# Optimization experiments

Hardware: AMD Instinct MI355X
Metric: run time of the kernel (lower is better)

Reference implementation:

```python
import jax, jax.numpy as jnp
import numpy as np

NUM_HEADS = 8
WS1, WS2 = 3, 5
SR = 8
RES = 56
DIM = 256


def _normalize(x, axis=-1, eps=1e-12):
    n = jnp.linalg.norm(x, axis=axis, keepdims=True)
    return x / jnp.maximum(n, eps)


def _unfold(img, ws):
    # img: (B, C, H, W) -> (B, C, ws*ws, H*W), torch nn.Unfold ordering
    B, C, H, W = img.shape
    p = ws // 2
    pad = jnp.pad(img, ((0, 0), (0, 0), (p, p), (p, p)))
    cols = jnp.stack([pad[:, :, i:i + H, j:j + W]
                      for i in range(ws) for j in range(ws)], axis=2)
    return cols.reshape(B, C, ws * ws, H * W)


def _local_mask(H, W, ws):
    # True where the unfolded window position falls on zero padding; shape (N, ws*ws)
    ones = jnp.ones((1, 1, H, W), jnp.float32)
    cols = _unfold(ones, ws)[0, 0]            # (ws*ws, N)
    return cols.T == 0                         # (N, ws*ws)


def _layernorm(x, g, b, eps=1e-5):
    mu = x.mean(-1, keepdims=True)
    var = ((x - mu) ** 2).mean(-1, keepdims=True)
    return (x - mu) * jax.lax.rsqrt(var + eps) * g + b


def setup_inputs() -> dict:
    key = jax.random.key(0)
    ks = jax.random.split(key, 8)
    C, B, N = DIM, 4, RES * RES
    hd = C // NUM_HEADS

    def nrm(k, shape, s=0.02):
        return jax.random.normal(k, shape, jnp.float32) * s

    return {
        "x": jax.random.normal(ks[0], (B, N, C), jnp.float32),
        "Wq": nrm(ks[1], (C, C)), "bq": jnp.zeros((C,), jnp.float32),
        "Wkv": nrm(ks[2], (C, 2 * C)), "bkv": jnp.zeros((2 * C,), jnp.float32),
        "Wsr": nrm(ks[3], (C, C)), "bsr": jnp.zeros((C,), jnp.float32),
        "ln_g": jnp.ones((C,), jnp.float32), "ln_b": jnp.zeros((C,), jnp.float32),
        "tok1": nrm(ks[4], (NUM_HEADS, hd, WS1 * WS1)),
        "bias1": jnp.zeros((NUM_HEADS, 1, WS1 * WS1), jnp.float32),
        "tok2": nrm(ks[5], (NUM_HEADS, hd, WS2 * WS2)),
        "bias2": jnp.zeros((NUM_HEADS, 1, WS2 * WS2), jnp.float32),
        "Wproj": nrm(ks[6], (C, C)), "bproj": jnp.zeros((C,), jnp.float32),
        "patch_size": 56,
    }


def reference(x, Wq, bq, Wkv, bkv, Wsr, bsr, ln_g, ln_b,
              tok1, bias1, tok2, bias2, Wproj, bproj, patch_size):
    H = W = int(patch_size)
    B, N, C = x.shape
    h = NUM_HEADS
    d = C // h
    l1, l2 = WS1 * WS1, WS2 * WS2

    # queries, cosine-normalized per head
    q = (x @ Wq + bq).reshape(B, N, h, d).transpose(0, 2, 1, 3)   # (B,h,N,d)
    qn = _normalize(q)

    # shared kv projection (torch computes it twice with identical result)
    kv = x @ Wkv + bkv
    k, v = kv[..., :C], kv[..., C:]
    kn = _normalize(k.reshape(B, N, h, d)).reshape(B, N, C)
    kv_img = jnp.concatenate([kn, v], axis=-1).transpose(0, 2, 1).reshape(B, 2 * C, H, W)

    def local_branch(ws):
        l = ws * ws
        cols = _unfold(kv_img, ws)                                # (B,2C,l,N)
        cols = cols.reshape(B, 2 * h, d, l, N).transpose(0, 1, 4, 2, 3)  # (B,2h,N,d,l)
        kl, vl = cols[:, :h], cols[:, h:]
        a = jnp.einsum('bhnd,bhndl->bhnl', qn, kl)
        a = jnp.where(_local_mask(H, W, ws)[None, None], -jnp.inf, a)
        return a, vl

    a1, vl1 = local_branch(WS1)
    a2, vl2 = local_branch(WS2)

    # pooled global branch
    x_img = x.transpose(0, 2, 1).reshape(B, C, H, W)
    x_sr = jnp.einsum('bchw,oc->bohw', x_img, Wsr.T.T) if False else jnp.einsum('bchw,co->bohw', x_img, Wsr) + bsr[None, :, None, None]
    x_sr = jax.nn.gelu(x_sr, approximate=False)
    pH, pW = H // SR, W // SR
    pooled = x_sr.reshape(B, C, pH, SR, pW, SR).mean(axis=(3, 5))  # adaptive avg pool
    P = pH * pW
    x_p = pooled.reshape(B, C, P).transpose(0, 2, 1)               # (B,P,C)
    x_p = _layernorm(x_p, ln_g, ln_b)
    kvp = (x_p @ Wkv + bkv).reshape(B, P, 2 * h, d).transpose(0, 2, 1, 3)
    kp, vp = kvp[:, :h], kvp[:, h:]
    ap = jnp.einsum('bhnd,bhpd->bhnp', qn, _normalize(kp))

    # joint softmax over both local windows and pooled tokens
    attn = jax.nn.softmax(jnp.concatenate([a1, a2, ap], axis=-1), axis=-1)
    s1 = attn[..., :l1]
    s2 = attn[..., l1:l1 + l2]
    sp = attn[..., l1 + l2:]

    x1 = jnp.einsum('bhnl,bhndl->bhnd',
                    jnp.einsum('bhnd,hdl->bhnl', qn, tok1) + bias1[None] + s1, vl1)
    x2 = jnp.einsum('bhnl,bhndl->bhnd',
                    jnp.einsum('bhnd,hdl->bhnl', qn, tok2) + bias2[None] + s2, vl2)
    xp = jnp.einsum('bhnp,bhpd->bhnd', sp, vp)

    out = (x1 + x2 + xp).transpose(0, 2, 1, 3).reshape(B, N, C)
    return out @ Wproj + bproj
```

## Files before the change

kernel.cpp:

```cpp
#include <hip/hip_runtime.h>
#include <hip/hip_bf16.h>

using bf16 = __hip_bfloat16;

#define B_  4
#define H_  56
#define W_  56
#define N_  3136
#define C_  256
#define NH  8
#define HD  32
#define P_  49
#define PH  7
#define TOKC 272
#define KS2  136

typedef __attribute__((ext_vector_type(8))) short short8;
typedef __attribute__((ext_vector_type(4))) float f32x4;

__device__ __forceinline__ float bfu2f(ushort u) { return __uint_as_float((uint32_t)u << 16); }
__device__ __forceinline__ ushort f2bf_u(float f) {
    uint32_t u = __float_as_uint(f);
    uint32_t r = (u + 0x7FFFu + ((u >> 16) & 1u)) >> 16;
    return (ushort)r;
}
__device__ __forceinline__ uint32_t pk2(float a, float b) {
    return (uint32_t)f2bf_u(a) | ((uint32_t)f2bf_u(b) << 16);
}
__device__ __forceinline__ float lo16(uint32_t u) { return __uint_as_float(u << 16); }
__device__ __forceinline__ float hi16(uint32_t u) { return __uint_as_float(u & 0xffff0000u); }

__device__ __forceinline__ float half_reduce(float v) {
#pragma unroll
    for (int m = 16; m >= 1; m >>= 1) v += __shfl_xor(v, m);
    return v;
}

__device__ __forceinline__ float block_sum(float val, float* red) {
#pragma unroll
    for (int m = 32; m >= 1; m >>= 1) val += __shfl_xor(val, m);
    __syncthreads();
    if ((threadIdx.x & 63) == 0) red[threadIdx.x >> 6] = val;
    __syncthreads();
    return red[0] + red[1] + red[2] + red[3];
}

__global__ __launch_bounds__(256) void k_prep(
    const float* __restrict__ Wq, const float* __restrict__ Wkv,
    const float* __restrict__ Wsr, const float* __restrict__ Wproj,
    const float* __restrict__ tok1, const float* __restrict__ bias1,
    const float* __restrict__ tok2, const float* __restrict__ bias2,
    ushort* __restrict__ WT, ushort* __restrict__ WTp,
    ushort* __restrict__ TD, float* __restrict__ biasT)
{
    const int gid = blockIdx.x * 256 + threadIdx.x;
    const int gs = gridDim.x * 256;
    for (int i = gid; i < 1024 * 256; i += gs) {
        int o = i >> 8, c = i & 255;
        float w = (o < 256) ? Wq[c * 256 + o]
                : (o < 768) ? Wkv[c * 512 + (o - 256)]
                            : Wsr[c * 256 + (o - 768)];
        WT[i] = f2bf_u(w);
    }
    for (int i = gid; i < 256 * 256; i += gs) {
        int o = i >> 8, c = i & 255;
        WTp[i] = f2bf_u(Wproj[c * 256 + o]);
    }
    for (int i = gid; i < 320 * 256; i += gs) {
        int j = i >> 8, k = i & 255;
        float val = 0.f;
        if (j < TOKC) {
            int h = j / 34, l = j % 34;
            if ((k >> 5) == h) {
                int d = k & 31;
                val = (l < 9) ? tok1[(h * HD + d) * 9 + l]
                              : tok2[(h * HD + d) * 25 + (l - 9)];
            }
        }
        TD[i] = f2bf_u(val);
    }
    for (int i = gid; i < 320; i += gs) {
        float bv = 0.f;
        if (i < TOKC) {
            int h = i / 34, l = i % 34;
            bv = (l < 9) ? bias1[h * 9 + l] : bias2[h * 25 + (l - 9)];
        }
        biasT[i] = bv;
    }
}

__global__ __launch_bounds__(256) void k_gemm_in(
    const float* __restrict__ xf,
    const ushort* __restrict__ WT,
    const float* __restrict__ bq, const float* __restrict__ bkv,
    const float* __restrict__ bsr,
    ushort* __restrict__ qnu,
    ushort* __restrict__ knu, ushort* __restrict__ vu, ushort* __restrict__ srgu)
{
    const int r0 = blockIdx.x * 64;
    const int halfy = blockIdx.y;
    const int t = threadIdx.x;
    __shared__ __align__(16) ushort As[64 * 264];
    __shared__ __align__(16) ushort Bs[64 * 264];

#pragma unroll
    for (int i = 0; i < 8; i++) {
        int chunk = t + i * 256;
        int row = chunk >> 5, ks8 = (chunk & 31) * 8;
        const float* src = xf + (size_t)(r0 + row) * 256 + ks8;
        float4 f0 = *(const float4*)(src);
        float4 f1 = *(const float4*)(src + 4);
        uint4 o;
        o.x = pk2(f0.x, f0.y); o.y = pk2(f0.z, f0.w);
        o.z = pk2(f1.x, f1.y); o.w = pk2(f1.z, f1.w);
        *(uint4*)(As + row * 264 + ks8) = o;
    }
    __syncthreads();

    const int w = t >> 6, lane = t & 63;
    const int arow = w * 16 + (lane & 15);
    const int k0 = (lane >> 4) * 8;
    const int colq = lane & 15;
    const int rb = r0 + w * 16 + (lane >> 4) * 4;

    short8 areg[8];
#pragma unroll
    for (int kk = 0; kk < 8; kk++)
        areg[kk] = *(const short8*)(As + arow * 264 + kk * 32 + k0);

    for (int cc = 0; cc < 8; cc++) {
        const int cb = halfy * 512 + cc * 64;
        const int mode = cb >> 8;
        const int cm = cb & 255;

        __syncthreads();
#pragma unroll
        for (int i = 0; i < 8; i++) {
            int chunk = t + i * 256;
            int row = chunk >> 5, ks8 = (chunk & 31) * 8;
            *(uint4*)(Bs + row * 264 + ks8) =
                *(const uint4*)(WT + (size_t)(cb + row) * 256 + ks8);
        }
        __syncthreads();

        f32x4 acc[4];
#pragma unroll
        for (int ct = 0; ct < 4; ct++) acc[ct] = (f32x4){0.f, 0.f, 0.f, 0.f};
#pragma unroll
        for (int kk = 0; kk < 8; kk++) {
#pragma unroll
            for (int ct = 0; ct < 4; ct++) {
                short8 b = *(const short8*)(Bs + (ct * 16 + colq) * 264 + kk * 32 + k0);
                acc[ct] = __builtin_amdgcn_mfma_f32_16x16x32_bf16(areg[kk], b, acc[ct], 0, 0, 0);
            }
        }

        const float* bp = (mode == 0) ? bq : (mode == 1) ? bkv : (mode == 2) ? (bkv + 256) : bsr;
#pragma unroll
        for (int ct = 0; ct < 4; ct++) {
            float bv = bp[cm + ct * 16 + colq];
#pragma unroll
            for (int j = 0; j < 4; j++) acc[ct][j] += bv;
        }

        if (mode <= 1) {
#pragma unroll
            for (int hp = 0; hp < 2; hp++) {
#pragma unroll
                for (int j = 0; j < 4; j++) {
                    float ss = acc[2 * hp][j] * acc[2 * hp][j] + acc[2 * hp + 1][j] * acc[2 * hp + 1][j];
                    ss += __shfl_xor(ss, 1); ss += __shfl_xor(ss, 2);
                    ss += __shfl_xor(ss, 4); ss += __shfl_xor(ss, 8);
                    float inv = 1.0f / fmaxf(sqrtf(ss), 1e-12f);
                    acc[2 * hp][j] *= inv; acc[2 * hp + 1][j] *= inv;
                }
            }
        } else if (mode == 3) {
#pragma unroll
            for (int ct = 0; ct < 4; ct++)
#pragma unroll
                for (int j = 0; j < 4; j++) {
                    float s = acc[ct][j];
                    acc[ct][j] = 0.5f * s * (1.0f + erff(s * 0.70710678118654752f));
                }
        }

#pragma unroll
        for (int ct = 0; ct < 4; ct++) {
            int gcol = cm + ct * 16 + colq;
#pragma unroll
            for (int j = 0; j < 4; j++) {
                float vvv = acc[ct][j];
                size_t ro = (size_t)(rb + j);
                if (mode == 0)      qnu[ro * 256 + gcol] = f2bf_u(vvv);
                else if (mode == 1) knu[ro * 256 + gcol] = f2bf_u(vvv);
                else if (mode == 2) vu[ro * 256 + gcol] = f2bf_u(vvv);
                else                srgu[ro * 256 + gcol] = f2bf_u(vvv);
            }
        }
    }
}

template <int MODE>
__global__ __launch_bounds__(256) void k_gemm(
    const ushort* __restrict__ Abf,
    const ushort* __restrict__ WT,
    const float*  __restrict__ bias,
    float* __restrict__ dstF,
    ushort* __restrict__ dstT)
{
    const int r0 = blockIdx.x * 64;
    const int cb = blockIdx.y * 64;
    const int t = threadIdx.x;
    __shared__ __align__(16) ushort As[64 * 264];
    __shared__ __align__(16) ushort Bs[64 * 264];

#pragma unroll
    for (int i = 0; i < 8; i++) {
        int chunk = t + i * 256;
        int row = chunk >> 5, ks = (chunk & 31) * 8;
        *(uint4*)(As + row * 264 + ks) = *(const uint4*)(Abf + (size_t)(r0 + row) * 256 + ks);
        *(uint4*)(Bs + row * 264 + ks) = *(const uint4*)(WT + (size_t)(cb + row) * 256 + ks);
    }
    __syncthreads();

    const int w = t >> 6, lane = t & 63;
    const int arow = w * 16 + (lane & 15);
    const int k0 = (lane >> 4) * 8;
    f32x4 acc[4];
#pragma unroll
    for (int ct = 0; ct < 4; ct++) acc[ct] = (f32x4){0.f, 0.f, 0.f, 0.f};

#pragma unroll
    for (int kk = 0; kk < 8; kk++) {
        short8 a = *(const short8*)(As + arow * 264 + kk * 32 + k0);
#pragma unroll
        for (int ct = 0; ct < 4; ct++) {
            short8 b = *(const short8*)(Bs + (ct * 16 + (lane & 15)) * 264 + kk * 32 + k0);
            acc[ct] = __builtin_amdgcn_mfma_f32_16x16x32_bf16(a, b, acc[ct], 0, 0, 0);
        }
    }

    const int colq = lane & 15;
    const int rb = r0 + w * 16 + (lane >> 4) * 4;
#pragma unroll
    for (int ct = 0; ct < 4; ct++) {
        float bv = bias[cb + ct * 16 + colq];
#pragma unroll
        for (int j = 0; j < 4; j++) acc[ct][j] += bv;
    }

#pragma unroll
    for (int ct = 0; ct < 4; ct++) {
        int gcol = cb + ct * 16 + colq;
#pragma unroll
        for (int j = 0; j < 4; j++) {
            if (MODE == 4) {
                dstF[(size_t)(rb + j) * 256 + gcol] = acc[ct][j];
            } else {
                if (gcol < TOKC)
                    dstT[(size_t)(rb + j) * TOKC + gcol] = f2bf_u(acc[ct][j]);
            }
        }
    }
}

__global__ __launch_bounds__(256) void k_srt(
    const uint32_t* __restrict__ srgu32,
    const float* __restrict__ Wkv, const float* __restrict__ bkv,
    const float* __restrict__ ln_g, const float* __restrict__ ln_b,
    ushort* __restrict__ kpn_u, ushort* __restrict__ vpu)
{
    const int cell = blockIdx.x;
    const int b = cell / P_, p = cell % P_;
    const int py = p / PH, px = p % PH;
    const int t = threadIdx.x;
    const int ph = t >> 7, cp = t & 127;
    __shared__ float xp[C_];
    __shared__ float red[4];

    float sx = 0.f, sy = 0.f;
    for (int k = 0; k < 32; k++) {
        int pi = ph * 32 + k;
        int n = (py * 8 + (pi >> 3)) * W_ + px * 8 + (pi & 7);
        uint32_t u = srgu32[((size_t)b * N_ + n) * 128 + cp];
        sx += lo16(u); sy += hi16(u);
    }
    if (ph == 1) { xp[2 * cp] = sx; xp[2 * cp + 1] = sy; }
    __syncthreads();
    if (ph == 0) {
        xp[2 * cp]     = (xp[2 * cp] + sx) * (1.0f / 64.0f);
        xp[2 * cp + 1] = (xp[2 * cp + 1] + sy) * (1.0f / 64.0f);
    }
    __syncthreads();

    float acc = xp[t];
    float mean = block_sum(acc, red) * (1.0f / C_);
    float dv = acc - mean;
    float var = block_sum(dv * dv, red) * (1.0f / C_);
    float xpv = dv * rsqrtf(var + 1e-5f) * ln_g[t] + ln_b[t];
    __syncthreads();
    xp[t] = xpv;
    __syncthreads();

    float ak = bkv[t];
    float av = bkv[C_ + t];
    for (int c = 0; c < C_; c++) {
        float xv = xp[c];
        ak += xv * Wkv[c * 2 * C_ + t];
        av += xv * Wkv[c * 2 * C_ + C_ + t];
    }
    float nk = fmaxf(sqrtf(half_reduce(ak * ak)), 1e-12f);
    size_t o = (size_t)cell * C_ + t;
    kpn_u[o] = f2bf_u(ak / nk);
    vpu[o]  = f2bf_u(av);
}

__global__ __launch_bounds__(256) void k_qkav(
    const ushort* __restrict__ qnu,
    const uint32_t* __restrict__ knu,
    const uint32_t* __restrict__ vu,
    const ushort* __restrict__ kpnu,
    const ushort* __restrict__ vpu,
    const ushort* __restrict__ tokcu,
    uint32_t* __restrict__ pre_bfu)
{
    const int tile = blockIdx.x;
    const int b  = blockIdx.y >> 1;
    const int hs = blockIdx.y & 1;
    const int ty = tile / 14, tx = tile % 14;
    const int t = threadIdx.x;
    __shared__ __align__(16) ushort ks[64 * KS2];
    __shared__ ushort coefS[16 * 4 * 80];
    __shared__ ushort tokcS[16 * 136];

    uint32_t* ks32 = (uint32_t*)ks;
    for (int idx = t; idx < 64 * 32; idx += 256) {
        int r = idx >> 5, u2 = idx & 31;
        int gy = ty * 4 + (r >> 3) - 2, gx = tx * 4 + (r & 7) - 2;
        uint2 kv = make_uint2(0u, 0u);
        if (gy >= 0 && gy < H_ && gx >= 0 && gx < W_) {
            size_t base = ((size_t)b * N_ + gy * W_ + gx) * 128 + hs * 64 + 2 * u2;
            kv = *reinterpret_cast<const uint2*>(knu + base);
        }
        ks32[r * (KS2 / 2) + 2 * u2]     = kv.x;
        ks32[r * (KS2 / 2) + 2 * u2 + 1] = kv.y;
    }
    {
        uint32_t* tokcS32 = (uint32_t*)tokcS;
        const uint32_t* tsrc = (const uint32_t*)tokcu;
        for (int idx = t; idx < 16 * 68; idx += 256) {
            int tk = idx / 68, d = idx % 68;
            size_t flat = (size_t)b * N_ + (ty * 4 + (tk >> 2)) * W_ + tx * 4 + (tk & 3);
            tokcS32[tk * 68 + d] = tsrc[flat * 136 + hs * 68 + d];
        }
    }
    __syncthreads();

    const int w = t >> 6, lane = t & 63;
    const int h = hs * 4 + w;
    const int col = lane & 15, kslc = lane >> 4;

    int r8[4], c8[4]; bool inb[4]; int pcl[4]; bool pval[4];
#pragma unroll
    for (int ct = 0; ct < 4; ct++) {
        int key = ct * 16 + col;
        r8[ct] = key >> 3; c8[ct] = key & 7;
        int gy = ty * 4 + r8[ct] - 2, gx = tx * 4 + c8[ct] - 2;
        inb[ct] = (gy >= 0) && (gy < H_) && (gx >= 0) && (gx < W_);
        pval[ct] = key < P_;
        pcl[ct] = pval[ct] ? key : (P_ - 1);
    }

    size_t aflat = (size_t)b * N_ + (ty * 4 + (col >> 2)) * W_ + tx * 4 + (col & 3);
    short8 a = *(const short8*)(qnu + aflat * 256 + h * 32 + kslc * 8);

    f32x4 aw[4], ap[4];
#pragma unroll
    for (int ct = 0; ct < 4; ct++) {
        short8 bw = *(const short8*)(ks + (ct * 16 + col) * KS2 + w * 32 + kslc * 8);
        aw[ct] = __builtin_amdgcn_mfma_f32_16x16x32_bf16(a, bw, (f32x4){0.f,0.f,0.f,0.f}, 0, 0, 0);
        short8 bp = *(const short8*)(kpnu + ((size_t)b * P_ + pcl[ct]) * 256 + h * 32 + kslc * 8);
        ap[ct] = __builtin_amdgcn_mfma_f32_16x16x32_bf16(a, bp, (f32x4){0.f,0.f,0.f,0.f}, 0, 0, 0);
    }

#pragma unroll
    for (int j = 0; j < 4; j++) {
        float mj = -INFINITY;
#pragma unroll
        for (int ct = 0; ct < 4; ct++) {
            int dy = r8[ct] - kslc - 2, dx = c8[ct] - j - 2;
            bool win = inb[ct] && dy >= -2 && dy <= 2 && dx >= -2 && dx <= 2;
            if (win) mj = fmaxf(mj, aw[ct][j]);
            if (pval[ct]) mj = fmaxf(mj, ap[ct][j]);
        }
        mj = fmaxf(mj, __shfl_xor(mj, 1)); mj = fmaxf(mj, __shfl_xor(mj, 2));
        mj = fmaxf(mj, __shfl_xor(mj, 4)); mj = fmaxf(mj, __shfl_xor(mj, 8));
        float ej = 0.f;
        float ew[4], ep[4];
#pragma unroll
        for (int ct = 0; ct < 4; ct++) {
            int dy = r8[ct] - kslc - 2, dx = c8[ct] - j - 2;
            bool win = inb[ct] && dy >= -2 && dy <= 2 && dx >= -2 && dx <= 2;
            bool inner = dy >= -1 && dy <= 1 && dx >= -1 && dx <= 1;
            ew[ct] = win ? (inner ? 2.0f : 1.0f) * __expf(aw[ct][j] - mj) : 0.f;
            ep[ct] = pval[ct] ? __expf(ap[ct][j] - mj) : 0.f;
            ej += ew[ct] + ep[ct];
        }
        ej += __shfl_xor(ej, 1); ej += __shfl_xor(ej, 2);
        ej += __shfl_xor(ej, 4); ej += __shfl_xor(ej, 8);
        float sc = 1.0f / ej;
        const ushort* tokc_j = tokcS + (kslc * 4 + j) * 136 + w * 34;
        ushort* coefT = coefS + ((kslc * 4 + j) * 4 + w) * 80;
#pragma unroll
        for (int ct = 0; ct < 4; ct++) {
            int dy = r8[ct] - kslc - 2, dx = c8[ct] - j - 2;
            if (dy >= -2 && dy <= 2 && dx >= -2 && dx <= 2) {
                bool inner = dy >= -1 && dy <= 1 && dx >= -1 && dx <= 1;
                int l25 = (dy + 2) * 5 + (dx + 2);
                float tm = bfu2f(tokc_j[9 + l25]);
                if (inner) tm += bfu2f(tokc_j[(dy + 1) * 3 + (dx + 1)]);
                coefT[l25] = f2bf_u(ew[ct] * sc + tm);
            }
            if (pval[ct]) coefT[25 + ct * 16 + col] = f2bf_u(ep[ct] * sc);
        }
    }
    __syncthreads();

    const int tk = t >> 4, g = t & 15;
    const int iy = tk >> 2, ix = tk & 3;
    const int y = ty * 4 + iy, x = tx * 4 + ix;
    const size_t pflat = (size_t)b * N_ + y * W_ + x;
    const ushort* cf = coefS + (tk * 4 + (g >> 2)) * 80;

    float a0x = 0.f, a0y = 0.f, a1x = 0.f, a1y = 0.f;
    float a2x = 0.f, a2y = 0.f, a3x = 0.f, a3y = 0.f;

#pragma unroll 5
    for (int l = 0; l < 25; l++) {
        int dy = l / 5 - 2, dx = l % 5 - 2;
        int yy = y + dy, xx2 = x + dx;
        if (yy < 0 || yy >= H_ || xx2 < 0 || xx2 >= W_) continue;
        float wc = bfu2f(cf[l]);
        uint4 vv = *reinterpret_cast<const uint4*>(
            vu + ((size_t)b * N_ + yy * W_ + xx2) * 128 + hs * 64 + g * 4);
        a0x += wc * lo16(vv.x); a0y += wc * hi16(vv.x);
        a1x += wc * lo16(vv.y); a1y += wc * hi16(vv.y);
        a2x += wc * lo16(vv.z); a2y += wc * hi16(vv.z);
        a3x += wc * lo16(vv.w); a3y += wc * hi16(vv.w);
    }
#pragma unroll 7
    for (int p = 0; p < 49; p++) {
        float wc = bfu2f(cf[25 + p]);
        uint4 vv = *reinterpret_cast<const uint4*>(
            (const uint32_t*)vpu + ((size_t)b * P_ + p) * 128 + hs * 64 + g * 4);
        a0x += wc * lo16(vv.x); a0y += wc * hi16(vv.x);
        a1x += wc * lo16(vv.y); a1y += wc * hi16(vv.y);
        a2x += wc * lo16(vv.z); a2y += wc * hi16(vv.z);
        a3x += wc * lo16(vv.w); a3y += wc * hi16(vv.w);
    }
    uint4 o;
    o.x = pk2(a0x, a0y);
    o.y = pk2(a1x, a1y);
    o.z = pk2(a2x, a2y);
    o.w = pk2(a3x, a3y);
    *reinterpret_cast<uint4*>(pre_bfu + pflat * 128 + hs * 64 + g * 4) = o;
}

extern "C" void kernel_launch(void* const* d_in, const int* in_sizes, int n_in,
                              void* d_out, int out_size, void* d_ws, size_t ws_size,
                              hipStream_t stream)
{
    (void)in_sizes; (void)n_in; (void)out_size; (void)ws_size;
    const float* x     = (const float*)d_in[0];
    const float* Wq    = (const float*)d_in[1];
    const float* bq    = (const float*)d_in[2];
    const float* Wkv   = (const float*)d_in[3];
    const float* bkv   = (const float*)d_in[4];
    const float* Wsr   = (const float*)d_in[5];
    const float* bsr   = (const float*)d_in[6];
    const float* ln_g  = (const float*)d_in[7];
    const float* ln_b  = (const float*)d_in[8];
    const float* tok1  = (const float*)d_in[9];
    const float* bias1 = (const float*)d_in[10];
    const float* tok2  = (const float*)d_in[11];
    const float* bias2 = (const float*)d_in[12];
    const float* Wproj = (const float*)d_in[13];
    const float* bproj = (const float*)d_in[14];
    float* out = (float*)d_out;

    const size_t nhalf = (size_t)B_ * N_ * 128;

    uint32_t* vu     = (uint32_t*)d_ws;
    uint32_t* knu    = vu + nhalf;
    uint32_t* srgu   = knu + nhalf;
    uint32_t* qnu32  = srgu + nhalf;
    ushort*   WTus   = (ushort*)(qnu32 + nhalf);
    ushort*   WTpus  = WTus + 1024 * 256;
    ushort*   TDus   = WTpus + 256 * 256;
    float*    biasT  = (float*)(TDus + 320 * 256);
    ushort*   vpu    = (ushort*)(biasT + 320);
    uint32_t* kpnu   = (uint32_t*)(vpu + (size_t)B_ * P_ * 256);

    ushort* qnu   = (ushort*)qnu32;
    ushort* tokcu = (ushort*)d_out;

    k_prep<<<512, 256, 0, stream>>>(Wq, Wkv, Wsr, Wproj, tok1, bias1, tok2, bias2,
                                    WTus, WTpus, TDus, biasT);
    k_gemm_in<<<dim3(196, 2), 256, 0, stream>>>(x, WTus, bq, bkv, bsr,
                                                qnu, (ushort*)knu,
                                                (ushort*)vu, (ushort*)srgu);
    k_gemm<5><<<dim3(196, 5), 256, 0, stream>>>(qnu, TDus, biasT, nullptr, tokcu);
    k_srt<<<B_ * P_, 256, 0, stream>>>(srgu, Wkv, bkv, ln_g, ln_b, (ushort*)kpnu, vpu);
    k_qkav<<<dim3(196, B_ * 2), 256, 0, stream>>>(qnu, knu, vu, (const ushort*)kpnu,
                                                  vpu, tokcu, srgu);
    k_gemm<4><<<dim3(196, 4), 256, 0, stream>>>((ushort*)srgu, WTpus, bproj, out, nullptr);
}
```

Baseline: 128.6 us.

## Compute attention-weighted V aggregation with MFMA using padded channel-major V layout

The scalar per-thread gather of 25 local V neighbours and 49 pooled V tokens is replaced by MFMA matrix multiplies. V is now stored channel-major in a zero-padded spatial grid, and pooled V is stored transposed and padded to 64. This lets coefficient tiles in shared memory multiply against contiguous V rows. The aim is to cut scalar FMA and uncoalesced-load cost in the aggregation step. In exchange, the prep kernel must zero a large padded buffer and the V write in the GEMM epilogue becomes strided scatter.

```diff
diff --git a/kernel.cpp b/kernel.cpp
--- a/kernel.cpp
+++ b/kernel.cpp
@@ -14,9 +14,14 @@
 #define PH  7
 #define TOKC 272
 #define KS2  136
+#define CPAD 80
+#define VTH  60
+#define VTW  64
 
 typedef __attribute__((ext_vector_type(8))) short short8;
 typedef __attribute__((ext_vector_type(4))) float f32x4;
+
+union U8 { uint4 u; short8 s; };
 
 __device__ __forceinline__ float bfu2f(ushort u) { return __uint_as_float((uint32_t)u << 16); }
 __device__ __forceinline__ ushort f2bf_u(float f) {
@@ -51,7 +56,8 @@
     const float* __restrict__ tok1, const float* __restrict__ bias1,
     const float* __restrict__ tok2, const float* __restrict__ bias2,
     ushort* __restrict__ WT, ushort* __restrict__ WTp,
-    ushort* __restrict__ TD, float* __restrict__ biasT)
+    ushort* __restrict__ TD, float* __restrict__ biasT,
+    uint32_t* __restrict__ vT32, uint32_t* __restrict__ vpT32)
 {
     const int gid = blockIdx.x * 256 + threadIdx.x;
     const int gs = gridDim.x * 256;
@@ -87,6 +93,9 @@
         }
         biasT[i] = bv;
     }
+    const int nvt = B_ * 256 * VTH * VTW / 2;
+    for (int i = gid; i < nvt; i += gs) vT32[i] = 0u;
+    for (int i = gid; i < B_ * 256 * 32; i += gs) vpT32[i] = 0u;
 }
 
 __global__ __launch_bounds__(256) void k_gemm_in(
@@ -95,7 +104,7 @@
     const float* __restrict__ bq, const float* __restrict__ bkv,
     const float* __restrict__ bsr,
     ushort* __restrict__ qnu,
-    ushort* __restrict__ knu, ushort* __restrict__ vu, ushort* __restrict__ srgu)
+    ushort* __restrict__ knu, ushort* __restrict__ vT, ushort* __restrict__ srgu)
 {
     const int r0 = blockIdx.x * 64;
     const int halfy = blockIdx.y;
@@ -194,8 +203,13 @@
                 size_t ro = (size_t)(rb + j);
                 if (mode == 0)      qnu[ro * 256 + gcol] = f2bf_u(vvv);
                 else if (mode == 1) knu[ro * 256 + gcol] = f2bf_u(vvv);
-                else if (mode == 2) vu[ro * 256 + gcol] = f2bf_u(vvv);
-                else                srgu[ro * 256 + gcol] = f2bf_u(vvv);
+                else if (mode == 2) {
+                    int bb = (int)(ro / N_), n = (int)(ro % N_);
+                    int yy = n / W_, xx = n % W_;
+                    vT[((size_t)(bb * 256 + gcol) * VTH + yy + 2) * VTW + xx + 2] = f2bf_u(vvv);
+                } else {
+                    srgu[ro * 256 + gcol] = f2bf_u(vvv);
+                }
             }
         }
     }
@@ -269,7 +283,7 @@
     const uint32_t* __restrict__ srgu32,
     const float* __restrict__ Wkv, const float* __restrict__ bkv,
     const float* __restrict__ ln_g, const float* __restrict__ ln_b,
-    ushort* __restrict__ kpn_u, ushort* __restrict__ vpu)
+    ushort* __restrict__ kpn_u, ushort* __restrict__ vpT)
 {
     const int cell = blockIdx.x;
     const int b = cell / P_, p = cell % P_;
@@ -311,38 +325,39 @@
         av += xv * Wkv[c * 2 * C_ + C_ + t];
     }
     float nk = fmaxf(sqrtf(half_reduce(ak * ak)), 1e-12f);
-    size_t o = (size_t)cell * C_ + t;
-    kpn_u[o] = f2bf_u(ak / nk);
-    vpu[o]  = f2bf_u(av);
+    kpn_u[(size_t)cell * C_ + t] = f2bf_u(ak / nk);
+    vpT[((size_t)b * 256 + t) * 64 + p] = f2bf_u(av);
 }
 
 __global__ __launch_bounds__(256) void k_qkav(
     const ushort* __restrict__ qnu,
     const uint32_t* __restrict__ knu,
-    const uint32_t* __restrict__ vu,
     const ushort* __restrict__ kpnu,
-    const ushort* __restrict__ vpu,
     const ushort* __restrict__ tokcu,
-    uint32_t* __restrict__ pre_bfu)
+    const ushort* __restrict__ vT,
+    const ushort* __restrict__ vpT,
+    ushort* __restrict__ preu)
 {
     const int tile = blockIdx.x;
     const int b  = blockIdx.y >> 1;
     const int hs = blockIdx.y & 1;
     const int ty = tile / 14, tx = tile % 14;
     const int t = threadIdx.x;
-    __shared__ __align__(16) ushort ks[64 * KS2];
-    __shared__ ushort coefS[16 * 4 * 80];
+
+    __shared__ __align__(16) ushort shmem[2 * 4 * 16 * CPAD];
     __shared__ ushort tokcS[16 * 136];
+    ushort* ks = shmem;
+    ushort* coefW = shmem;
+    ushort* coefP = shmem + 4 * 16 * CPAD;
 
     uint32_t* ks32 = (uint32_t*)ks;
     for (int idx = t; idx < 64 * 32; idx += 256) {
         int r = idx >> 5, u2 = idx & 31;
         int gy = ty * 4 + (r >> 3) - 2, gx = tx * 4 + (r & 7) - 2;
         uint2 kv = make_uint2(0u, 0u);
-        if (gy >= 0 && gy < H_ && gx >= 0 && gx < W_) {
-            size_t base = ((size_t)b * N_ + gy * W_ + gx) * 128 + hs * 64 + 2 * u2;
-            kv = *reinterpret_cast<const uint2*>(knu + base);
-        }
+        if (gy >= 0 && gy < H_ && gx >= 0 && gx < W_)
+            kv = *reinterpret_cast<const uint2*>(
+                knu + ((size_t)b * N_ + gy * W_ + gx) * 128 + hs * 64 + 2 * u2);
         ks32[r * (KS2 / 2) + 2 * u2]     = kv.x;
         ks32[r * (KS2 / 2) + 2 * u2 + 1] = kv.y;
     }
@@ -384,6 +399,8 @@
         ap[ct] = __builtin_amdgcn_mfma_f32_16x16x32_bf16(a, bp, (f32x4){0.f,0.f,0.f,0.f}, 0, 0, 0);
     }
 
+    __syncthreads();
+
 #pragma unroll
     for (int j = 0; j < 4; j++) {
         float mj = -INFINITY;
@@ -411,60 +428,52 @@
         ej += __shfl_xor(ej, 4); ej += __shfl_xor(ej, 8);
         float sc = 1.0f / ej;
         const ushort* tokc_j = tokcS + (kslc * 4 + j) * 136 + w * 34;
-        ushort* coefT = coefS + ((kslc * 4 + j) * 4 + w) * 80;
+        const int trow = (w * 16 + kslc * 4 + j) * CPAD;
 #pragma unroll
         for (int ct = 0; ct < 4; ct++) {
             int dy = r8[ct] - kslc - 2, dx = c8[ct] - j - 2;
+            float cw = 0.f;
             if (dy >= -2 && dy <= 2 && dx >= -2 && dx <= 2) {
                 bool inner = dy >= -1 && dy <= 1 && dx >= -1 && dx <= 1;
                 int l25 = (dy + 2) * 5 + (dx + 2);
                 float tm = bfu2f(tokc_j[9 + l25]);
                 if (inner) tm += bfu2f(tokc_j[(dy + 1) * 3 + (dx + 1)]);
-                coefT[l25] = f2bf_u(ew[ct] * sc + tm);
+                cw = ew[ct] * sc + tm;
             }
-            if (pval[ct]) coefT[25 + ct * 16 + col] = f2bf_u(ep[ct] * sc);
-        }
-    }
-    __syncthreads();
-
-    const int tk = t >> 4, g = t & 15;
-    const int iy = tk >> 2, ix = tk & 3;
-    const int y = ty * 4 + iy, x = tx * 4 + ix;
-    const size_t pflat = (size_t)b * N_ + y * W_ + x;
-    const ushort* cf = coefS + (tk * 4 + (g >> 2)) * 80;
-
-    float a0x = 0.f, a0y = 0.f, a1x = 0.f, a1y = 0.f;
-    float a2x = 0.f, a2y = 0.f, a3x = 0.f, a3y = 0.f;
-
-#pragma unroll 5
-    for (int l = 0; l < 25; l++) {
-        int dy = l / 5 - 2, dx = l % 5 - 2;
-        int yy = y + dy, xx2 = x + dx;
-        if (yy < 0 || yy >= H_ || xx2 < 0 || xx2 >= W_) continue;
-        float wc = bfu2f(cf[l]);
-        uint4 vv = *reinterpret_cast<const uint4*>(
-            vu + ((size_t)b * N_ + yy * W_ + xx2) * 128 + hs * 64 + g * 4);
-        a0x += wc * lo16(vv.x); a0y += wc * hi16(vv.x);
-        a1x += wc * lo16(vv.y); a1y += wc * hi16(vv.y);
-        a2x += wc * lo16(vv.z); a2y += wc * hi16(vv.z);
-        a3x += wc * lo16(vv.w); a3y += wc * hi16(vv.w);
-    }
-#pragma unroll 7
-    for (int p = 0; p < 49; p++) {
-        float wc = bfu2f(cf[25 + p]);
-        uint4 vv = *reinterpret_cast<const uint4*>(
-            (const uint32_t*)vpu + ((size_t)b * P_ + p) * 128 + hs * 64 + g * 4);
-        a0x += wc * lo16(vv.x); a0y += wc * hi16(vv.x);
-        a1x += wc * lo16(vv.y); a1y += wc * hi16(vv.y);
-        a2x += wc * lo16(vv.z); a2y += wc * hi16(vv.z);
-        a3x += wc * lo16(vv.w); a3y += wc * hi16(vv.w);
-    }
-    uint4 o;
-    o.x = pk2(a0x, a0y);
-    o.y = pk2(a1x, a1y);
-    o.z = pk2(a2x, a2y);
-    o.w = pk2(a3x, a3y);
-    *reinterpret_cast<uint4*>(pre_bfu + pflat * 128 + hs * 64 + g * 4) = o;
+            coefW[trow + ct * 16 + col] = f2bf_u(cw);
+            coefP[trow + ct * 16 + col] = f2bf_u(pval[ct] ? ep[ct] * sc : 0.f);
+        }
+    }
+    __syncthreads();
+
+    f32x4 accO[2];
+    accO[0] = (f32x4){0.f,0.f,0.f,0.f};
+    accO[1] = (f32x4){0.f,0.f,0.f,0.f};
+#pragma unroll
+    for (int kc = 0; kc < 2; kc++) {
+        short8 aWf = *(const short8*)(coefW + (w * 16 + col) * CPAD + kc * 32 + kslc * 8);
+        short8 aPf = *(const short8*)(coefP + (w * 16 + col) * CPAD + kc * 32 + kslc * 8);
+#pragma unroll
+        for (int ct = 0; ct < 2; ct++) {
+            int chg = hs * 128 + w * 32 + ct * 16 + col;
+            size_t vbase = (((size_t)(b * 256 + chg)) * VTH + ty * 4 + kc * 4 + kslc) * VTW + tx * 4;
+            uint2 l0 = *(const uint2*)(vT + vbase);
+            uint2 l1 = *(const uint2*)(vT + vbase + 4);
+            U8 ub; ub.u = make_uint4(l0.x, l0.y, l1.x, l1.y);
+            accO[ct] = __builtin_amdgcn_mfma_f32_16x16x32_bf16(aWf, ub.s, accO[ct], 0, 0, 0);
+            short8 bPf = *(const short8*)(vpT + ((size_t)b * 256 + chg) * 64 + kc * 32 + kslc * 8);
+            accO[ct] = __builtin_amdgcn_mfma_f32_16x16x32_bf16(aPf, bPf, accO[ct], 0, 0, 0);
+        }
+    }
+#pragma unroll
+    for (int ct = 0; ct < 2; ct++) {
+        int chg = hs * 128 + w * 32 + ct * 16 + col;
+#pragma unroll
+        for (int j = 0; j < 4; j++) {
+            size_t pflat = (size_t)b * N_ + (ty * 4 + kslc) * W_ + tx * 4 + j;
+            preu[pflat * 256 + chg] = f2bf_u(accO[ct][j]);
+        }
+    }
 }
 
 extern "C" void kernel_launch(void* const* d_in, const int* in_sizes, int n_in,
@@ -490,29 +499,30 @@
     float* out = (float*)d_out;
 
     const size_t nhalf = (size_t)B_ * N_ * 128;
-
-    uint32_t* vu     = (uint32_t*)d_ws;
-    uint32_t* knu    = vu + nhalf;
+    const size_t nvt   = (size_t)B_ * 256 * VTH * VTW;
+
+    uint32_t* knu    = (uint32_t*)d_ws;
     uint32_t* srgu   = knu + nhalf;
     uint32_t* qnu32  = srgu + nhalf;
-    ushort*   WTus   = (ushort*)(qnu32 + nhalf);
+    ushort*   vTus   = (ushort*)(qnu32 + nhalf);
+    ushort*   WTus   = vTus + nvt;
     ushort*   WTpus  = WTus + 1024 * 256;
     ushort*   TDus   = WTpus + 256 * 256;
     float*    biasT  = (float*)(TDus + 320 * 256);
-    ushort*   vpu    = (ushort*)(biasT + 320);
-    uint32_t* kpnu   = (uint32_t*)(vpu + (size_t)B_ * P_ * 256);
+    ushort*   vpTus  = (ushort*)(biasT + 320);
+    ushort*   kpnuS  = vpTus + (size_t)B_ * 256 * 64;
 
     ushort* qnu   = (ushort*)qnu32;
     ushort* tokcu = (ushort*)d_out;
 
     k_prep<<<512, 256, 0, stream>>>(Wq, Wkv, Wsr, Wproj, tok1, bias1, tok2, bias2,
-                                    WTus, WTpus, TDus, biasT);
+                                    WTus, WTpus, TDus, biasT,
+                                    (uint32_t*)vTus, (uint32_t*)vpTus);
     k_gemm_in<<<dim3(196, 2), 256, 0, stream>>>(x, WTus, bq, bkv, bsr,
-                                                qnu, (ushort*)knu,
-                                                (ushort*)vu, (ushort*)srgu);
+                                                qnu, (ushort*)knu, vTus, (ushort*)srgu);
     k_gemm<5><<<dim3(196, 5), 256, 0, stream>>>(qnu, TDus, biasT, nullptr, tokcu);
-    k_srt<<<B_ * P_, 256, 0, stream>>>(srgu, Wkv, bkv, ln_g, ln_b, (ushort*)kpnu, vpu);
-    k_qkav<<<dim3(196, B_ * 2), 256, 0, stream>>>(qnu, knu, vu, (const ushort*)kpnu,
-                                                  vpu, tokcu, srgu);
+    k_srt<<<B_ * P_, 256, 0, stream>>>(srgu, Wkv, bkv, ln_g, ln_b, kpnuS, vpTus);
+    k_qkav<<<dim3(196, B_ * 2), 256, 0, stream>>>(qnu, knu, kpnuS, tokcu,
+                                                  vTus, vpTus, (ushort*)srgu);
     k_gemm<4><<<dim3(196, 4), 256, 0, stream>>>((ushort*)srgu, WTpus, bproj, out, nullptr);
 }
```

Result: faster. 114.7 us (-10.8%).
